# Optimization experiments

Measured on AMD Instinct MI355X. Metric: run time of the kernel, lower is better.

The kernel has to match this reference:

```python
import jax, jax.numpy as jnp
import numpy as np

D_MODEL = 1024
H = 16
D_H = D_MODEL // H
B = 8
S = 1024
NEG_INF = -1e9


def setup_inputs() -> dict:
    key = jax.random.key(0)
    ks = jax.random.split(key, 8)
    Qs = jax.random.normal(ks[0], (B, S, D_MODEL), dtype=jnp.float32)
    Ks = jax.random.normal(ks[1], (B, S, D_MODEL), dtype=jnp.float32)
    Vs = jax.random.normal(ks[2], (B, S, D_MODEL), dtype=jnp.float32)
    mask_3d = jnp.zeros((B, S, S), dtype=bool)
    # Parameters: torch.rand -> uniform[0,1) for per-head projections
    W_Q = jax.random.uniform(ks[3], (H, D_MODEL, D_H), dtype=jnp.float32)
    W_K = jax.random.uniform(ks[4], (H, D_MODEL, D_H), dtype=jnp.float32)
    W_V = jax.random.uniform(ks[5], (H, D_MODEL, D_H), dtype=jnp.float32)
    # Output nn.Linear(h*d_h, d_model): weight [d_model, h*d_h], bias [d_model]
    lim = 1.0 / np.sqrt(H * D_H)
    W_out = jax.random.uniform(ks[6], (D_MODEL, H * D_H), minval=-lim, maxval=lim, dtype=jnp.float32)
    b_out = jax.random.uniform(ks[7], (D_MODEL,), minval=-lim, maxval=lim, dtype=jnp.float32)
    return {"Qs": Qs, "Ks": Ks, "Vs": Vs, "mask_3d": mask_3d,
            "W_Q": W_Q, "W_K": W_K, "W_V": W_V, "W_out": W_out, "b_out": b_out}


def reference(Qs, Ks, Vs, mask_3d, W_Q, W_K, W_V, W_out, b_out):
    # Fused per-head projections: avoid the explicit repeat in the torch code.
    q = jnp.einsum('bsk,hkl->bhsl', Qs, W_Q)  # [B,H,S,D_H]
    k = jnp.einsum('bsk,hkl->bhsl', Ks, W_K)
    v = jnp.einsum('bsk,hkl->bhsl', Vs, W_V)
    scale = 1.0 / jnp.sqrt(jnp.asarray(D_H, dtype=q.dtype))
    scores = jnp.einsum('bhqd,bhkd->bhqk', q, k) * scale  # [B,H,S,S]
    scores = jnp.where(mask_3d[:, None, :, :], NEG_INF, scores)
    attn = jax.nn.softmax(scores, axis=-1)
    out = jnp.einsum('bhqk,bhkd->bhqd', attn, v)  # [B,H,S,D_H]
    # chunk along head-batch dim then cat along feature dim == head-major concat
    out = jnp.transpose(out, (0, 2, 1, 3)).reshape(B, S, H * D_H)
    return out @ W_out.T + b_out
```

## Files before the change

kernel.cpp:

```cpp
#include <hip/hip_runtime.h>

#define DM 1024
#define H_ 16
#define DH 64
#define B_ 8
#define S_ 1024

typedef _Float16 half8 __attribute__((ext_vector_type(8)));
typedef _Float16 half4 __attribute__((ext_vector_type(4)));
typedef __fp16 fp16x2 __attribute__((ext_vector_type(2)));
typedef float f32x4 __attribute__((ext_vector_type(4)));
typedef float f32x16 __attribute__((ext_vector_type(16)));
typedef unsigned int uint;

static __device__ __forceinline__ uint pkrtz(float a, float b) {
    fp16x2 h = __builtin_amdgcn_cvt_pkrtz(a, b);
    return __builtin_bit_cast(uint, h);
}
#define PSWAP(d, s) asm volatile("v_permlane32_swap_b32 %0, %1" : "+v"(d), "+v"(s))

static __device__ __forceinline__ void gload16(const _Float16* g, _Float16* l) {
    __builtin_amdgcn_global_load_lds(
        (const __attribute__((address_space(1))) unsigned int*)(const void*)g,
        (__attribute__((address_space(3))) unsigned int*)(void*)l,
        16, 0, 0);
}

__global__ __launch_bounds__(256) void prep_k(
    const float* __restrict__ WQ, const float* __restrict__ WK,
    const float* __restrict__ WV, const float* __restrict__ WO,
    const unsigned char* __restrict__ mask,
    _Float16* __restrict__ wqh, _Float16* __restrict__ wql,
    _Float16* __restrict__ wkh, _Float16* __restrict__ wkl,
    _Float16* __restrict__ wv,  _Float16* __restrict__ wo,
    unsigned char* __restrict__ scan)
{
    __shared__ __align__(16) _Float16 Lh[64][72];
    __shared__ __align__(16) _Float16 Ll[64][72];
    __shared__ int s_red[4];
    const int t = threadIdx.x;
    const int blk = blockIdx.x;

    if (blk < 256) {
        const int kb = blk & 15;
        const int h  = blk >> 4;
        #pragma unroll
        for (int s = 0; s < 3; ++s) {
            const float* W = (s == 0) ? WQ : ((s == 1) ? WK : WV);
            const int krow = t >> 2, lc = t & 3;
            const float* rp = W + (((size_t)h * 1024 + kb * 64 + krow) * 64 + lc * 16);
            #pragma unroll
            for (int q4 = 0; q4 < 4; ++q4) {
                float4 f = ((const float4*)rp)[q4];
                float vv0 = f.x, vv1 = f.y, vv2 = f.z, vv3 = f.w;
                int l0 = lc * 16 + q4 * 4;
                _Float16 h0 = (_Float16)vv0; Lh[l0 + 0][krow] = h0; Ll[l0 + 0][krow] = (_Float16)(vv0 - (float)h0);
                _Float16 h1 = (_Float16)vv1; Lh[l0 + 1][krow] = h1; Ll[l0 + 1][krow] = (_Float16)(vv1 - (float)h1);
                _Float16 h2 = (_Float16)vv2; Lh[l0 + 2][krow] = h2; Ll[l0 + 2][krow] = (_Float16)(vv2 - (float)h2);
                _Float16 h3 = (_Float16)vv3; Lh[l0 + 3][krow] = h3; Ll[l0 + 3][krow] = (_Float16)(vv3 - (float)h3);
            }
            __syncthreads();
            const int l = t >> 2, pc = t & 3;
            #pragma unroll
            for (int hp = 0; hp < 2; ++hp) {
                int p = pc + 4 * hp;
                int lc2 = p ^ (l & 7);
                half8 vh = *(const half8*)&Lh[l][lc2 * 8];
                half8 vl = *(const half8*)&Ll[l][lc2 * 8];
                size_t off = (size_t)(h * 64 + l) * DM + kb * 64 + p * 8;
                if (s == 0) { *(half8*)(wqh + off) = vh; *(half8*)(wql + off) = vl; }
                else if (s == 1) { *(half8*)(wkh + off) = vh; *(half8*)(wkl + off) = vl; }
                else { *(half8*)(wv + off) = vh; }
            }
            __syncthreads();
        }
    } else if (blk < 768) {
        int idx8 = (blk - 256) * 256 + t;
        int n = idx8 >> 7;
        int c = idx8 & 127;
        int p = (c & ~7) | ((c & 7) ^ (n & 7));
        const float* rp = WO + ((size_t)n * DM + c * 8);
        float4 a = ((const float4*)rp)[0];
        float4 b = ((const float4*)rp)[1];
        half8 v;
        v[0] = (_Float16)a.x; v[1] = (_Float16)a.y; v[2] = (_Float16)a.z; v[3] = (_Float16)a.w;
        v[4] = (_Float16)b.x; v[5] = (_Float16)b.y; v[6] = (_Float16)b.z; v[7] = (_Float16)b.w;
        *(half8*)(wo + (size_t)n * DM + p * 8) = v;
    } else {
        const int g = blk - 768;
        const int q64 = g & 15, k64 = (g >> 4) & 15, b = g >> 8;
        uint4 mv = *(const uint4*)(mask + ((size_t)b * S_ + q64 * 64 + (t >> 2)) * S_ + k64 * 64 + (t & 3) * 16);
        int a = (mv.x | mv.y | mv.z | mv.w) != 0;
        unsigned long long bal = __ballot(a);
        if ((t & 63) == 0) s_red[t >> 6] = (bal != 0ull);
        __syncthreads();
        if (t == 0)
            scan[(b * 16 + q64) * 16 + k64] =
                (unsigned char)(s_red[0] | s_red[1] | s_red[2] | s_red[3]);
    }
}

__global__ __launch_bounds__(512) void gemm_split_k(
    const float* __restrict__ A0, const float* __restrict__ A1,
    const _Float16* __restrict__ Bh0, const _Float16* __restrict__ Bl0,
    const _Float16* __restrict__ Bh1, const _Float16* __restrict__ Bl1,
    _Float16* __restrict__ Chi0, _Float16* __restrict__ Clo0,
    _Float16* __restrict__ Chi1, _Float16* __restrict__ Clo1)
{
    const int lid = blockIdx.x + 8 * blockIdx.y + 512 * blockIdx.z;
    const int xcd = lid & 7, k2 = lid >> 3;
    const int G = xcd * 16 + (k2 >> 3);
    const int bxv = k2 & 7, byv = G & 63, z = G >> 6;

    const float* A = z ? A1 : A0;
    const _Float16* Bh = z ? Bh1 : Bh0;
    const _Float16* Bl = z ? Bl1 : Bl0;
    _Float16* Chi = z ? Chi1 : Chi0;
    _Float16* Clo = z ? Clo1 : Clo0;

    __shared__ __align__(16) _Float16 SM[32768];
    _Float16* Ah  = SM;
    _Float16* Al  = SM + 8192;
    _Float16* Bhs = SM + 16384;
    _Float16* Bls = SM + 24576;

    const int t = threadIdx.x;
    const int lane = t & 63;
    const int w = t >> 6;
    const int wm = (w >> 1) * 32;
    const int wn = (w & 1) * 64;
    const int l15 = lane & 15;
    const int l4g = lane >> 4;

    const int bm = byv * 128;
    const int bn = bxv * 128;

    f32x4 acc[2][4] = {};

    float4 ar[4];
    auto aload = [&](int KT) {
        #pragma unroll
        for (int i = 0; i < 4; ++i)
            ar[i] = *(const float4*)(A + (size_t)(bm + (t >> 4) + 32 * i) * DM + KT * 64 + (t & 15) * 4);
    };
    auto awr = [&]() {
        #pragma unroll
        for (int i = 0; i < 4; ++i) {
            int row = (t >> 4) + 32 * i;
            int c4 = t & 15;
            float4 v = ar[i];
            half4 hv, lv;
            hv[0] = (_Float16)v.x; lv[0] = (_Float16)(v.x - (float)hv[0]);
            hv[1] = (_Float16)v.y; lv[1] = (_Float16)(v.y - (float)hv[1]);
            hv[2] = (_Float16)v.z; lv[2] = (_Float16)(v.z - (float)hv[2]);
            hv[3] = (_Float16)v.w; lv[3] = (_Float16)(v.w - (float)hv[3]);
            int off = row * 64 + (((c4 >> 1) ^ (row & 7)) * 8) + (c4 & 1) * 4;
            *(half4*)&Ah[off] = hv;
            *(half4*)&Al[off] = lv;
        }
    };
    auto bgl = [&](int KT) {
        #pragma unroll
        for (int jj = 0; jj < 2; ++jj) {
            int rr = w * 16 + jj * 8 + (lane >> 3);
            const size_t so = (size_t)(bn + rr) * DM + KT * 64 + (lane & 7) * 8;
            gload16(Bh + so, &Bhs[(w * 16 + jj * 8) * 64]);
            gload16(Bl + so, &Bls[(w * 16 + jj * 8) * 64]);
        }
    };

    aload(0);
    bgl(0);
    for (int kt = 0; kt < 16; ++kt) {
        awr();
        __syncthreads();
        if (kt < 15) aload(kt + 1);
        #pragma unroll
        for (int ks = 0; ks < 2; ++ks) {
            half8 ah[2], al[2], bh[4], bl[4];
            const int slotx = (ks * 4 + l4g);
            #pragma unroll
            for (int mi = 0; mi < 2; ++mi) {
                int r = wm + mi * 16 + l15;
                int off = r * 64 + (slotx ^ (l15 & 7)) * 8;
                ah[mi] = *(const half8*)&Ah[off];
                al[mi] = *(const half8*)&Al[off];
            }
            #pragma unroll
            for (int ni = 0; ni < 4; ++ni) {
                int r = wn + ni * 16 + l15;
                int off = r * 64 + (slotx ^ (l15 & 7)) * 8;
                bh[ni] = *(const half8*)&Bhs[off];
                bl[ni] = *(const half8*)&Bls[off];
            }
            #pragma unroll
            for (int mi = 0; mi < 2; ++mi)
                #pragma unroll
                for (int ni = 0; ni < 4; ++ni) {
                    acc[mi][ni] = __builtin_amdgcn_mfma_f32_16x16x32_f16(ah[mi], bh[ni], acc[mi][ni], 0, 0, 0);
                    acc[mi][ni] = __builtin_amdgcn_mfma_f32_16x16x32_f16(ah[mi], bl[ni], acc[mi][ni], 0, 0, 0);
                    acc[mi][ni] = __builtin_amdgcn_mfma_f32_16x16x32_f16(al[mi], bh[ni], acc[mi][ni], 0, 0, 0);
                }
        }
        __syncthreads();
        if (kt < 15) bgl(kt + 1);
    }

    #pragma unroll
    for (int mi = 0; mi < 2; ++mi)
        #pragma unroll
        for (int ni = 0; ni < 4; ++ni) {
            int col = bn + wn + ni * 16 + l15;
            #pragma unroll
            for (int r = 0; r < 4; ++r) {
                int row = bm + wm + mi * 16 + l4g * 4 + r;
                float val = acc[mi][ni][r];
                _Float16 hv = (_Float16)val;
                Chi[(size_t)row * DM + col] = hv;
                Clo[(size_t)row * DM + col] = (_Float16)(val - (float)hv);
            }
        }
}

__global__ __launch_bounds__(256) void gemm_v_k(
    const float* __restrict__ A, const _Float16* __restrict__ Bt,
    _Float16* __restrict__ C)
{
    const int lid = blockIdx.x + 8 * blockIdx.y;
    const int xcd = lid & 7, k2 = lid >> 3;
    const int G = xcd * 8 + (k2 >> 3);
    const int bxv = k2 & 7, byv = G;

    __shared__ __align__(16) _Float16 SM[25600];
    _Float16* As  = SM;
    _Float16* Bsb = SM + 9216;

    const int t = threadIdx.x;
    const int lane = t & 63;
    const int w = t >> 6;
    const int wm = (w >> 1) * 64;
    const int wn = (w & 1) * 64;
    const int l15 = lane & 15;
    const int l4g = lane >> 4;

    const int bm = byv * 128;
    const int bn = bxv * 128;

    f32x4 acc[4][4] = {};

    const int arow = t >> 4, ac4 = t & 15;
    float4 ar[8];
    auto aload = [&](int KT) {
        #pragma unroll
        for (int i = 0; i < 8; ++i)
            ar[i] = *(const float4*)(A + (size_t)(bm + arow + 16 * i) * DM + KT * 64 + ac4 * 4);
    };
    auto awr = [&]() {
        #pragma unroll
        for (int i = 0; i < 8; ++i) {
            float4 v = ar[i];
            half4 hv;
            hv[0] = (_Float16)v.x; hv[1] = (_Float16)v.y;
            hv[2] = (_Float16)v.z; hv[3] = (_Float16)v.w;
            *(half4*)&As[(arow + 16 * i) * 72 + ac4 * 4] = hv;
        }
    };
    auto bgl = [&](int KT, int buf) {
        _Float16* Bd = Bsb + buf * 8192;
        #pragma unroll
        for (int jj = 0; jj < 4; ++jj) {
            int rr = w * 32 + jj * 8 + (lane >> 3);
            gload16(Bt + (size_t)(bn + rr) * DM + KT * 64 + (lane & 7) * 8,
                    &Bd[(w * 32 + jj * 8) * 64]);
        }
    };

    aload(0);
    bgl(0, 0);
    for (int kt = 0; kt < 16; ++kt) {
        const _Float16* Bcur = Bsb + (kt & 1) * 8192;
        awr();
        __syncthreads();
        if (kt < 15) { aload(kt + 1); bgl(kt + 1, (kt + 1) & 1); }
        #pragma unroll
        for (int ks = 0; ks < 2; ++ks) {
            half8 a[4], b[4];
            #pragma unroll
            for (int mi = 0; mi < 4; ++mi)
                a[mi] = *(const half8*)&As[(wm + mi * 16 + l15) * 72 + ks * 32 + l4g * 8];
            #pragma unroll
            for (int ni = 0; ni < 4; ++ni) {
                int row = wn + ni * 16 + l15;
                int slot = (ks * 4 + l4g) ^ (l15 & 7);
                b[ni] = *(const half8*)&Bcur[row * 64 + slot * 8];
            }
            #pragma unroll
            for (int mi = 0; mi < 4; ++mi)
                #pragma unroll
                for (int ni = 0; ni < 4; ++ni)
                    acc[mi][ni] = __builtin_amdgcn_mfma_f32_16x16x32_f16(a[mi], b[ni], acc[mi][ni], 0, 0, 0);
        }
        __syncthreads();
    }

    _Float16* Tw = SM + w * 4608;
    #pragma unroll
    for (int mi = 0; mi < 4; ++mi)
        #pragma unroll
        for (int ni = 0; ni < 4; ++ni)
            #pragma unroll
            for (int r = 0; r < 4; ++r)
                Tw[(ni * 16 + l15) * 72 + mi * 16 + l4g * 4 + r] = (_Float16)acc[mi][ni][r];
    __syncthreads();
    {
        const int mg0 = bm + wm;
        const int b = mg0 >> 10, s0 = mg0 & 1023;
        _Float16* op = C + ((size_t)b * DM + (bn + wn + lane)) * S_ + s0;
        #pragma unroll
        for (int c8 = 0; c8 < 8; ++c8)
            *(half8*)(op + c8 * 8) = *(const half8*)&Tw[lane * 72 + c8 * 8];
    }
}

__global__ __launch_bounds__(256) void gemm_out_k(
    const _Float16* __restrict__ A, const _Float16* __restrict__ Bt,
    float* __restrict__ C, const float* __restrict__ bias)
{
    const int lid = blockIdx.x + 8 * blockIdx.y;
    const int xcd = lid & 7, k2 = lid >> 3;
    const int G = xcd * 8 + (k2 >> 3);
    const int bxv = k2 & 7, byv = G;

    __shared__ __align__(16) _Float16 SM[25600];
    _Float16* As  = SM;
    _Float16* Bsb = SM + 9216;

    const int t = threadIdx.x;
    const int lane = t & 63;
    const int w = t >> 6;
    const int wm = (w >> 1) * 64;
    const int wn = (w & 1) * 64;
    const int l15 = lane & 15;
    const int l4g = lane >> 4;

    const int bm = byv * 128;
    const int bn = bxv * 128;

    f32x4 acc[4][4] = {};

    uint4 arr[4];
    auto aload = [&](int KT) {
        #pragma unroll
        for (int i = 0; i < 4; ++i)
            arr[i] = *(const uint4*)(A + (size_t)(bm + (t >> 3) + 32 * i) * DM + KT * 64 + (t & 7) * 8);
    };
    auto awr = [&]() {
        #pragma unroll
        for (int i = 0; i < 4; ++i)
            *(uint4*)&As[((t >> 3) + 32 * i) * 72 + (t & 7) * 8] = arr[i];
    };
    auto bgl = [&](int KT, int buf) {
        _Float16* Bd = Bsb + buf * 8192;
        #pragma unroll
        for (int jj = 0; jj < 4; ++jj) {
            int rr = w * 32 + jj * 8 + (lane >> 3);
            gload16(Bt + (size_t)(bn + rr) * DM + KT * 64 + (lane & 7) * 8,
                    &Bd[(w * 32 + jj * 8) * 64]);
        }
    };

    aload(0);
    bgl(0, 0);
    for (int kt = 0; kt < 16; ++kt) {
        const _Float16* Bcur = Bsb + (kt & 1) * 8192;
        awr();
        __syncthreads();
        if (kt < 15) { aload(kt + 1); bgl(kt + 1, (kt + 1) & 1); }
        #pragma unroll
        for (int ks = 0; ks < 2; ++ks) {
            half8 a[4], b[4];
            #pragma unroll
            for (int mi = 0; mi < 4; ++mi)
                a[mi] = *(const half8*)&As[(wm + mi * 16 + l15) * 72 + ks * 32 + l4g * 8];
            #pragma unroll
            for (int ni = 0; ni < 4; ++ni) {
                int row = wn + ni * 16 + l15;
                int slot = (ks * 4 + l4g) ^ (l15 & 7);
                b[ni] = *(const half8*)&Bcur[row * 64 + slot * 8];
            }
            #pragma unroll
            for (int mi = 0; mi < 4; ++mi)
                #pragma unroll
                for (int ni = 0; ni < 4; ++ni)
                    acc[mi][ni] = __builtin_amdgcn_mfma_f32_16x16x32_f16(a[mi], b[ni], acc[mi][ni], 0, 0, 0);
        }
        __syncthreads();
    }

    #pragma unroll
    for (int mi = 0; mi < 4; ++mi)
        #pragma unroll
        for (int ni = 0; ni < 4; ++ni) {
            int col = bn + wn + ni * 16 + l15;
            #pragma unroll
            for (int r = 0; r < 4; ++r) {
                int row = bm + wm + mi * 16 + l4g * 4 + r;
                C[(size_t)row * DM + col] = acc[mi][ni][r] + bias[col];
            }
        }
}

__global__ __launch_bounds__(256) void attn_k(
    const _Float16* __restrict__ qhg, const _Float16* __restrict__ qlg,
    const _Float16* __restrict__ khg, const _Float16* __restrict__ klg,
    const _Float16* __restrict__ vtg, const unsigned char* __restrict__ maskg,
    const unsigned char* __restrict__ scanp, _Float16* __restrict__ ho)
{
    __shared__ __align__(16) _Float16 Kh[64][72];
    __shared__ __align__(16) _Float16 Kl[64][72];
    __shared__ __align__(16) _Float16 Vt[64][72];

    const int t = threadIdx.x;
    const int lane = t & 63;
    const int w = t >> 6;
    const int l31 = lane & 31;
    const int hi = lane >> 5;

    const int j = blockIdx.y + 16 * blockIdx.z;
    const int head = 16 * blockIdx.x + (j >> 3);
    const int qt = j & 7;
    const int h = head & 15;
    const int b = head >> 4;

    const int colbase = h * DH;
    const int qrow = qt * 128 + w * 32 + l31;

    half8 qfh[4], qfl[4];
    {
        const size_t base = ((size_t)b * S_ + qrow) * DM + colbase;
        #pragma unroll
        for (int ds = 0; ds < 4; ++ds) {
            qfh[ds] = *(const half8*)(qhg + base + ds * 16 + hi * 8);
            qfl[ds] = *(const half8*)(qlg + base + ds * 16 + hi * 8);
        }
    }

    float m_q = -1e30f, ls = 0.0f;
    f32x16 accO0 = {};
    f32x16 accO1 = {};

    const int r0 = t >> 3;
    const int c0 = (t & 7) * 8;
    const _Float16* kph = khg + ((size_t)b * S_) * DM + colbase;
    const _Float16* kpl = klg + ((size_t)b * S_) * DM + colbase;
    const _Float16* vp  = vtg + ((size_t)b * DM + colbase) * S_;
    const unsigned char* sc0 = scanp + (b * 16 + 2 * qt) * 16;
    const unsigned char* sc1 = scanp + (b * 16 + 2 * qt + 1) * 16;

    uint4 akh0, akh1, akl0, akl1, av0, av1;
#define ALOAD(KT) do { \
        akh0 = *(const uint4*)(kph + (size_t)((KT) * 64 + r0) * DM + c0);       \
        akh1 = *(const uint4*)(kph + (size_t)((KT) * 64 + 32 + r0) * DM + c0);  \
        akl0 = *(const uint4*)(kpl + (size_t)((KT) * 64 + r0) * DM + c0);       \
        akl1 = *(const uint4*)(kpl + (size_t)((KT) * 64 + 32 + r0) * DM + c0);  \
        av0  = *(const uint4*)(vp + (size_t)r0 * S_ + (KT) * 64 + c0);          \
        av1  = *(const uint4*)(vp + (size_t)(32 + r0) * S_ + (KT) * 64 + c0);   \
    } while (0)
#define AWRITE() do { \
        *(uint4*)&Kh[r0][c0] = akh0; *(uint4*)&Kh[32 + r0][c0] = akh1; \
        *(uint4*)&Kl[r0][c0] = akl0; *(uint4*)&Kl[32 + r0][c0] = akl1; \
        *(uint4*)&Vt[r0][c0] = av0;  *(uint4*)&Vt[32 + r0][c0] = av1;  \
    } while (0)

    ALOAD(0);
    AWRITE();
    int msk = sc0[0] | sc1[0];

    const float SC = 0.125f * 1.44269504089f;
    const float THRRAW = 8.0f / SC;

    for (int kt = 0; kt < 16; ++kt) {
        __syncthreads();
        const int mskcur = msk;
        if (kt < 15) {
            ALOAD(kt + 1);
            msk = sc0[kt + 1] | sc1[kt + 1];
        }

        f32x16 sa0 = {}, sa1 = {};
        __builtin_amdgcn_s_setprio(1);
        #pragma unroll
        for (int ds = 0; ds < 4; ++ds) {
            half8 kh0 = *(const half8*)&Kh[l31][ds * 16 + hi * 8];
            half8 kl0 = *(const half8*)&Kl[l31][ds * 16 + hi * 8];
            half8 kh1 = *(const half8*)&Kh[32 + l31][ds * 16 + hi * 8];
            half8 kl1 = *(const half8*)&Kl[32 + l31][ds * 16 + hi * 8];
            sa0 = __builtin_amdgcn_mfma_f32_32x32x16_f16(kh0, qfh[ds], sa0, 0, 0, 0);
            sa0 = __builtin_amdgcn_mfma_f32_32x32x16_f16(kh0, qfl[ds], sa0, 0, 0, 0);
            sa0 = __builtin_amdgcn_mfma_f32_32x32x16_f16(kl0, qfh[ds], sa0, 0, 0, 0);
            sa1 = __builtin_amdgcn_mfma_f32_32x32x16_f16(kh1, qfh[ds], sa1, 0, 0, 0);
            sa1 = __builtin_amdgcn_mfma_f32_32x32x16_f16(kh1, qfl[ds], sa1, 0, 0, 0);
            sa1 = __builtin_amdgcn_mfma_f32_32x32x16_f16(kl1, qfh[ds], sa1, 0, 0, 0);
        }
        __builtin_amdgcn_s_setprio(0);

        if (mskcur) {
            const unsigned char* mrow = maskg + ((size_t)b * S_ + qrow) * S_ + kt * 64;
            #pragma unroll
            for (int e = 0; e < 16; ++e) {
                int kl_ = (e & 3) + 8 * (e >> 2) + 4 * hi;
                if (mrow[kl_]) sa0[e] = -1e9f;
                if (mrow[32 + kl_]) sa1[e] = -1e9f;
            }
        }

        float rm = fmaxf(sa0[0], sa0[1]);
        #pragma unroll
        for (int e = 2; e < 16; e += 2) rm = fmaxf(fmaxf(rm, sa0[e]), sa0[e + 1]);
        #pragma unroll
        for (int e = 0; e < 16; e += 2) rm = fmaxf(fmaxf(rm, sa1[e]), sa1[e + 1]);
        rm = fmaxf(rm, __shfl_xor(rm, 32));
        if (__any(rm > m_q + THRRAW)) {
            const float mn = fmaxf(m_q, rm);
            const float sfac = exp2f((m_q - mn) * SC);
            m_q = mn;
            ls *= sfac;
            #pragma unroll
            for (int e = 0; e < 16; ++e) { accO0[e] *= sfac; accO1[e] *= sfac; }
        }
        const float nmn = -m_q * SC;
        float rs = 0.0f;
        #pragma unroll
        for (int e = 0; e < 16; ++e) { sa0[e] = exp2f(fmaf(sa0[e], SC, nmn)); rs += sa0[e]; }
        #pragma unroll
        for (int e = 0; e < 16; ++e) { sa1[e] = exp2f(fmaf(sa1[e], SC, nmn)); rs += sa1[e]; }
        rs += __shfl_xor(rs, 32);
        ls += rs;

        half8 pf[4];
        {
            uint c0_ = pkrtz(sa0[0], sa0[1]),  c1_ = pkrtz(sa0[2], sa0[3]);
            uint c2_ = pkrtz(sa0[4], sa0[5]),  c3_ = pkrtz(sa0[6], sa0[7]);
            uint c4_ = pkrtz(sa0[8], sa0[9]),  c5_ = pkrtz(sa0[10], sa0[11]);
            uint c6_ = pkrtz(sa0[12], sa0[13]), c7_ = pkrtz(sa0[14], sa0[15]);
            PSWAP(c0_, c2_); PSWAP(c1_, c3_);
            PSWAP(c4_, c6_); PSWAP(c5_, c7_);
            uint4 u0 = {c0_, c1_, c2_, c3_}, u1 = {c4_, c5_, c6_, c7_};
            pf[0] = __builtin_bit_cast(half8, u0);
            pf[1] = __builtin_bit_cast(half8, u1);
        }
        {
            uint c0_ = pkrtz(sa1[0], sa1[1]),  c1_ = pkrtz(sa1[2], sa1[3]);
            uint c2_ = pkrtz(sa1[4], sa1[5]),  c3_ = pkrtz(sa1[6], sa1[7]);
            uint c4_ = pkrtz(sa1[8], sa1[9]),  c5_ = pkrtz(sa1[10], sa1[11]);
            uint c6_ = pkrtz(sa1[12], sa1[13]), c7_ = pkrtz(sa1[14], sa1[15]);
            PSWAP(c0_, c2_); PSWAP(c1_, c3_);
            PSWAP(c4_, c6_); PSWAP(c5_, c7_);
            uint4 u0 = {c0_, c1_, c2_, c3_}, u1 = {c4_, c5_, c6_, c7_};
            pf[2] = __builtin_bit_cast(half8, u0);
            pf[3] = __builtin_bit_cast(half8, u1);
        }
        __builtin_amdgcn_s_setprio(1);
        #pragma unroll
        for (int kc = 0; kc < 4; ++kc) {
            half8 vf0 = *(const half8*)&Vt[l31][kc * 16 + hi * 8];
            half8 vf1 = *(const half8*)&Vt[32 + l31][kc * 16 + hi * 8];
            accO0 = __builtin_amdgcn_mfma_f32_32x32x16_f16(vf0, pf[kc], accO0, 0, 0, 0);
            accO1 = __builtin_amdgcn_mfma_f32_32x32x16_f16(vf1, pf[kc], accO1, 0, 0, 0);
        }
        __builtin_amdgcn_s_setprio(0);

        __syncthreads();
        if (kt < 15) AWRITE();
    }
#undef ALOAD
#undef AWRITE

    const float inv = 1.0f / ls;
    _Float16* orow = ho + ((size_t)b * S_ + qrow) * DM + colbase;
    #pragma unroll
    for (int g2 = 0; g2 < 4; ++g2) {
        half4 hv0, hv1;
        #pragma unroll
        for (int e = 0; e < 4; ++e) {
            hv0[e] = (_Float16)(accO0[g2 * 4 + e] * inv);
            hv1[e] = (_Float16)(accO1[g2 * 4 + e] * inv);
        }
        *(half4*)(orow + g2 * 8 + hi * 4) = hv0;
        *(half4*)(orow + 32 + g2 * 8 + hi * 4) = hv1;
    }
}

extern "C" void kernel_launch(void* const* d_in, const int* in_sizes, int n_in,
                              void* d_out, int out_size, void* d_ws, size_t ws_size,
                              hipStream_t stream)
{
    const float* Qs = (const float*)d_in[0];
    const float* Ks = (const float*)d_in[1];
    const float* Vs = (const float*)d_in[2];
    const unsigned char* mask = (const unsigned char*)d_in[3];
    const float* WQ = (const float*)d_in[4];
    const float* WK = (const float*)d_in[5];
    const float* WV = (const float*)d_in[6];
    const float* WO = (const float*)d_in[7];
    const float* bo = (const float*)d_in[8];

    char* ws = (char*)d_ws;
    const size_t MB = 1024 * 1024;
    _Float16* wqh = (_Float16*)(ws + 0 * MB);
    _Float16* wql = (_Float16*)(ws + 2 * MB);
    _Float16* wkh = (_Float16*)(ws + 4 * MB);
    _Float16* wkl = (_Float16*)(ws + 6 * MB);
    _Float16* wv  = (_Float16*)(ws + 8 * MB);
    _Float16* wo  = (_Float16*)(ws + 10 * MB);
    _Float16* qhi = (_Float16*)(ws + 12 * MB);
    _Float16* qlo = (_Float16*)(ws + 28 * MB);
    _Float16* khi = (_Float16*)(ws + 44 * MB);
    _Float16* klo = (_Float16*)(ws + 60 * MB);
    _Float16* vt  = (_Float16*)(ws + 76 * MB);
    _Float16* hh  = (_Float16*)(ws + 92 * MB);
    unsigned char* scan = (unsigned char*)(ws + 108 * MB);

    prep_k<<<2816, 256, 0, stream>>>(WQ, WK, WV, WO, mask,
                                     wqh, wql, wkh, wkl, wv, wo, scan);

    gemm_split_k<<<dim3(8, 64, 2), 512, 0, stream>>>(
        Qs, Ks, wqh, wql, wkh, wkl, qhi, qlo, khi, klo);

    gemm_v_k<<<dim3(8, 64), 256, 0, stream>>>(Vs, wv, vt);

    attn_k<<<dim3(8, 16, 8), 256, 0, stream>>>(qhi, qlo, khi, klo, vt, mask, scan, hh);

    gemm_out_k<<<dim3(8, 64), 256, 0, stream>>>(hh, wo, (float*)d_out, bo);
}
```

Before: 298.8 us.

## Double-buffer attention LDS tiles and async-load swizzled A in output GEMM

The attention kernel now double-buffers its K-high, K-low and V tiles in shared memory. This drops one barrier per iteration, since the next tile is written into the other buffer. The attention output is stored with each head's 8-element chunks XOR-swizzled by row. That lets the output-projection GEMM load A directly into LDS with global_load_lds and read it back conflict-free through the same swizzle, removing the register staging step. The cost is higher LDS use in both kernels, which may lower occupancy, and a cross-kernel layout dependency that must stay consistent.

```diff
diff --git a/kernel.cpp b/kernel.cpp
--- a/kernel.cpp
+++ b/kernel.cpp
@@ -331,9 +331,7 @@
     const int G = xcd * 8 + (k2 >> 3);
     const int bxv = k2 & 7, byv = G;
 
-    __shared__ __align__(16) _Float16 SM[25600];
-    _Float16* As  = SM;
-    _Float16* Bsb = SM + 9216;
+    __shared__ __align__(16) _Float16 SM[32768];
 
     const int t = threadIdx.x;
     const int lane = t & 63;
@@ -348,45 +346,38 @@
 
     f32x4 acc[4][4] = {};
 
-    uint4 arr[4];
-    auto aload = [&](int KT) {
-        #pragma unroll
-        for (int i = 0; i < 4; ++i)
-            arr[i] = *(const uint4*)(A + (size_t)(bm + (t >> 3) + 32 * i) * DM + KT * 64 + (t & 7) * 8);
-    };
-    auto awr = [&]() {
-        #pragma unroll
-        for (int i = 0; i < 4; ++i)
-            *(uint4*)&As[((t >> 3) + 32 * i) * 72 + (t & 7) * 8] = arr[i];
-    };
-    auto bgl = [&](int KT, int buf) {
-        _Float16* Bd = Bsb + buf * 8192;
+    auto stage = [&](int KT, int buf) {
+        _Float16* Ad = SM + buf * 8192;
+        _Float16* Bd = SM + 16384 + buf * 8192;
         #pragma unroll
         for (int jj = 0; jj < 4; ++jj) {
             int rr = w * 32 + jj * 8 + (lane >> 3);
-            gload16(Bt + (size_t)(bn + rr) * DM + KT * 64 + (lane & 7) * 8,
-                    &Bd[(w * 32 + jj * 8) * 64]);
+            const size_t go = (size_t)rr * DM + KT * 64 + (lane & 7) * 8;
+            gload16(A + (size_t)bm * DM + go, Ad + (w * 32 + jj * 8) * 64);
+            gload16(Bt + (size_t)bn * DM + go, Bd + (w * 32 + jj * 8) * 64);
         }
     };
 
-    aload(0);
-    bgl(0, 0);
+    stage(0, 0);
+    __syncthreads();
     for (int kt = 0; kt < 16; ++kt) {
-        const _Float16* Bcur = Bsb + (kt & 1) * 8192;
-        awr();
-        __syncthreads();
-        if (kt < 15) { aload(kt + 1); bgl(kt + 1, (kt + 1) & 1); }
+        const int buf = kt & 1;
+        if (kt < 15) stage(kt + 1, buf ^ 1);
+        const _Float16* Ac = SM + buf * 8192;
+        const _Float16* Bc = SM + 16384 + buf * 8192;
         #pragma unroll
         for (int ks = 0; ks < 2; ++ks) {
             half8 a[4], b[4];
-            #pragma unroll
-            for (int mi = 0; mi < 4; ++mi)
-                a[mi] = *(const half8*)&As[(wm + mi * 16 + l15) * 72 + ks * 32 + l4g * 8];
+            const int slotx = ks * 4 + l4g;
+            #pragma unroll
+            for (int mi = 0; mi < 4; ++mi) {
+                int row = wm + mi * 16 + l15;
+                a[mi] = *(const half8*)&Ac[row * 64 + ((slotx ^ (l15 & 7)) * 8)];
+            }
             #pragma unroll
             for (int ni = 0; ni < 4; ++ni) {
                 int row = wn + ni * 16 + l15;
-                int slot = (ks * 4 + l4g) ^ (l15 & 7);
-                b[ni] = *(const half8*)&Bcur[row * 64 + slot * 8];
+                b[ni] = *(const half8*)&Bc[row * 64 + ((slotx ^ (l15 & 7)) * 8)];
             }
             #pragma unroll
             for (int mi = 0; mi < 4; ++mi)
@@ -416,9 +407,9 @@
     const _Float16* __restrict__ vtg, const unsigned char* __restrict__ maskg,
     const unsigned char* __restrict__ scanp, _Float16* __restrict__ ho)
 {
-    __shared__ __align__(16) _Float16 Kh[64][72];
-    __shared__ __align__(16) _Float16 Kl[64][72];
-    __shared__ __align__(16) _Float16 Vt[64][72];
+    __shared__ __align__(16) _Float16 KhB[2][64][72];
+    __shared__ __align__(16) _Float16 KlB[2][64][72];
+    __shared__ __align__(16) _Float16 VtB[2][64][72];
 
     const int t = threadIdx.x;
     const int lane = t & 63;
@@ -466,14 +457,14 @@
         av0  = *(const uint4*)(vp + (size_t)r0 * S_ + (KT) * 64 + c0);          \
         av1  = *(const uint4*)(vp + (size_t)(32 + r0) * S_ + (KT) * 64 + c0);   \
     } while (0)
-#define AWRITE() do { \
-        *(uint4*)&Kh[r0][c0] = akh0; *(uint4*)&Kh[32 + r0][c0] = akh1; \
-        *(uint4*)&Kl[r0][c0] = akl0; *(uint4*)&Kl[32 + r0][c0] = akl1; \
-        *(uint4*)&Vt[r0][c0] = av0;  *(uint4*)&Vt[32 + r0][c0] = av1;  \
+#define AWRITE(BUF) do { \
+        *(uint4*)&KhB[BUF][r0][c0] = akh0; *(uint4*)&KhB[BUF][32 + r0][c0] = akh1; \
+        *(uint4*)&KlB[BUF][r0][c0] = akl0; *(uint4*)&KlB[BUF][32 + r0][c0] = akl1; \
+        *(uint4*)&VtB[BUF][r0][c0] = av0;  *(uint4*)&VtB[BUF][32 + r0][c0] = av1;  \
     } while (0)
 
     ALOAD(0);
-    AWRITE();
+    AWRITE(0);
     int msk = sc0[0] | sc1[0];
 
     const float SC = 0.125f * 1.44269504089f;
@@ -481,6 +472,7 @@
 
     for (int kt = 0; kt < 16; ++kt) {
         __syncthreads();
+        const int cur = kt & 1;
         const int mskcur = msk;
         if (kt < 15) {
             ALOAD(kt + 1);
@@ -491,10 +483,10 @@
         __builtin_amdgcn_s_setprio(1);
         #pragma unroll
         for (int ds = 0; ds < 4; ++ds) {
-            half8 kh0 = *(const half8*)&Kh[l31][ds * 16 + hi * 8];
-            half8 kl0 = *(const half8*)&Kl[l31][ds * 16 + hi * 8];
-            half8 kh1 = *(const half8*)&Kh[32 + l31][ds * 16 + hi * 8];
-            half8 kl1 = *(const half8*)&Kl[32 + l31][ds * 16 + hi * 8];
+            half8 kh0 = *(const half8*)&KhB[cur][l31][ds * 16 + hi * 8];
+            half8 kl0 = *(const half8*)&KlB[cur][l31][ds * 16 + hi * 8];
+            half8 kh1 = *(const half8*)&KhB[cur][32 + l31][ds * 16 + hi * 8];
+            half8 kl1 = *(const half8*)&KlB[cur][32 + l31][ds * 16 + hi * 8];
             sa0 = __builtin_amdgcn_mfma_f32_32x32x16_f16(kh0, qfh[ds], sa0, 0, 0, 0);
             sa0 = __builtin_amdgcn_mfma_f32_32x32x16_f16(kh0, qfl[ds], sa0, 0, 0, 0);
             sa0 = __builtin_amdgcn_mfma_f32_32x32x16_f16(kl0, qfh[ds], sa0, 0, 0, 0);
@@ -563,21 +555,21 @@
         __builtin_amdgcn_s_setprio(1);
         #pragma unroll
         for (int kc = 0; kc < 4; ++kc) {
-            half8 vf0 = *(const half8*)&Vt[l31][kc * 16 + hi * 8];
-            half8 vf1 = *(const half8*)&Vt[32 + l31][kc * 16 + hi * 8];
+            half8 vf0 = *(const half8*)&VtB[cur][l31][kc * 16 + hi * 8];
+            half8 vf1 = *(const half8*)&VtB[cur][32 + l31][kc * 16 + hi * 8];
             accO0 = __builtin_amdgcn_mfma_f32_32x32x16_f16(vf0, pf[kc], accO0, 0, 0, 0);
             accO1 = __builtin_amdgcn_mfma_f32_32x32x16_f16(vf1, pf[kc], accO1, 0, 0, 0);
         }
         __builtin_amdgcn_s_setprio(0);
 
-        __syncthreads();
-        if (kt < 15) AWRITE();
+        if (kt < 15) AWRITE(cur ^ 1);
     }
 #undef ALOAD
 #undef AWRITE
 
     const float inv = 1.0f / ls;
     _Float16* orow = ho + ((size_t)b * S_ + qrow) * DM + colbase;
+    const int key = qrow & 7;
     #pragma unroll
     for (int g2 = 0; g2 < 4; ++g2) {
         half4 hv0, hv1;
@@ -586,8 +578,8 @@
             hv0[e] = (_Float16)(accO0[g2 * 4 + e] * inv);
             hv1[e] = (_Float16)(accO1[g2 * 4 + e] * inv);
         }
-        *(half4*)(orow + g2 * 8 + hi * 4) = hv0;
-        *(half4*)(orow + 32 + g2 * 8 + hi * 4) = hv1;
+        *(half4*)(orow + (g2 ^ key) * 8 + hi * 4) = hv0;
+        *(half4*)(orow + ((4 + g2) ^ key) * 8 + hi * 4) = hv1;
     }
 }
 
```

New measurement: 268.3 us. 1.11x faster.
